# Optimization experiments

Hardware: AMD Instinct MI355X
Metric: run time of the kernel (lower is better)

The kernel has to match this reference:

```python
import jax, jax.numpy as jnp
import numpy as np
import math

D = 512      # d_model
HEADS = 16   # num_heads
HD = 32      # head_dim
WS = 7       # window_size
KS = 8       # patch_size
S = 4        # spectral_stride


def dct_basis(n):
    k = np.arange(n, dtype=np.float64)[:, None]
    i = np.arange(n, dtype=np.float64)[None, :]
    B = np.cos(np.pi * (i + 0.5) * k / n)
    B[0, :] *= 1.0 / np.sqrt(2.0)
    B = B * np.sqrt(2.0 / n)
    return jnp.asarray(B, dtype=jnp.float32)


def setup_inputs() -> dict:
    key = jax.random.key(0)
    ks = jax.random.split(key, 24)
    Bb, H, W = 4, 112, 112
    N = H * W
    w = lambda k, shape: jax.random.normal(k, shape, jnp.float32) * 0.02
    return {
        'tokens': jax.random.normal(ks[0], (Bb, N, D), jnp.float32),
        'patches': jax.random.normal(ks[1], (Bb, 3 * KS * KS, N), jnp.float32),
        'Wq': w(ks[2], (D, D)), 'bq': w(ks[3], (D,)),
        'Wk': w(ks[4], (D, D)), 'bk': w(ks[5], (D,)),
        'Wv': w(ks[6], (D, D)), 'bv': w(ks[7], (D,)),
        'Wo': w(ks[8], (D, D)), 'bo': w(ks[9], (D,)),
        'Wsp': w(ks[10], (3 * KS * KS, D)), 'bsp': w(ks[11], (D,)),
        'Wsq': w(ks[12], (D, D)), 'bsq': w(ks[13], (D,)),
        'Wsk': w(ks[14], (D, D)), 'bsk': w(ks[15], (D,)),
        'Wsv': w(ks[16], (D, D)), 'bsv': w(ks[17], (D,)),
        'Wso': w(ks[18], (D, D)), 'bso': w(ks[19], (D,)),
        'alpha': jnp.asarray(0.5, jnp.float32),
        'H': H, 'W': W,
    }


def reference(tokens, patches, Wq, bq, Wk, bk, Wv, bv, Wo, bo,
              Wsp, bsp, Wsq, bsq, Wsk, bsk, Wsv, bsv, Wso, bso,
              alpha, H, W):
    B, N, d = tokens.shape
    # ---- local windowed multi-head attention ----
    ws = WS
    pad_h = (-H) % ws
    pad_w = (-W) % ws
    x = tokens.reshape(B, H, W, d)
    if pad_h or pad_w:
        x = jnp.pad(x, ((0, 0), (0, pad_h), (0, pad_w), (0, 0)))
    Hp, Wp = H + pad_h, W + pad_w
    nh, nw_ = Hp // ws, Wp // ws
    xw = x.reshape(B, nh, ws, nw_, ws, d).transpose(0, 1, 3, 2, 4, 5)
    xw = xw.reshape(B * nh * nw_, ws * ws, d)  # (nw, 49, d)
    nw, L, _ = xw.shape
    q = (xw @ Wq + bq).reshape(nw, L, HEADS, HD)
    k = (xw @ Wk + bk).reshape(nw, L, HEADS, HD)
    v = (xw @ Wv + bv).reshape(nw, L, HEADS, HD)
    scale = 1.0 / math.sqrt(HD)
    attn = jax.nn.softmax(jnp.einsum('nqhd,nkhd->nhqk', q, k) * scale, axis=-1)
    o = jnp.einsum('nhqk,nkhd->nqhd', attn, v).reshape(nw, L, d)
    o = o @ Wo + bo
    o = o.reshape(B, nh, nw_, ws, ws, d).transpose(0, 1, 3, 2, 4, 5).reshape(B, Hp, Wp, d)
    sp_out = o[:, :H, :W, :].reshape(B, N, d)
    # ---- DCT on raw patches -> spectral descriptors ----
    Bm = dct_basis(KS)
    p = patches.reshape(B, 3, KS, KS, N)
    Fc = jnp.einsum('ij,bcjkn->bcikn', Bm, p)
    Fc = jnp.einsum('bcijn,jk->bcikn', Fc, Bm)  # right-multiply by Bm^T transposed back
    spec_desc = Fc.reshape(B, 3 * KS * KS, N).transpose(0, 2, 1) @ Wsp + bsp  # (B,N,d)
    # ---- strided global spectral attention + nearest upsample ----
    spec_hw = spec_desc.reshape(B, H, W, d)
    sd = spec_hw[:, ::S, ::S, :]
    Hs, Ws = sd.shape[1], sd.shape[2]
    sd = sd.reshape(B, Hs * Ws, d)
    qs = sd @ Wsq + bsq
    ks_ = sd @ Wsk + bsk
    vs = sd @ Wsv + bsv
    a = jax.nn.softmax(jnp.einsum('bqd,bkd->bqk', qs, ks_) / math.sqrt(d), axis=-1)
    so = jnp.einsum('bqk,bkd->bqd', a, vs) @ Wso + bso
    so = so.reshape(B, Hs, Ws, d)
    ri = (jnp.arange(H) * Hs) // H  # torch nearest: floor(i*in/out)
    ci = (jnp.arange(W) * Ws) // W
    spec_out = so[:, ri][:, :, ci].reshape(B, N, d)
    # ---- fuse + residual + layernorm (no affine) ----
    al = jax.nn.sigmoid(alpha)
    out = tokens + al * sp_out + (1.0 - al) * spec_out
    mu = out.mean(-1, keepdims=True)
    var = ((out - mu) ** 2).mean(-1, keepdims=True)
    return (out - mu) / jnp.sqrt(var + 1e-5)
```

## Files before the change

kernel.cpp:

```cpp
#include <hip/hip_runtime.h>

typedef unsigned short u16;
typedef __attribute__((ext_vector_type(4))) float f32x4;
typedef __attribute__((ext_vector_type(8))) short bf16x8;

#define AS1 __attribute__((address_space(1)))
#define AS3 __attribute__((address_space(3)))
#define GLL(gp, lp) __builtin_amdgcn_global_load_lds((const AS1 void*)(gp), (AS3 void*)(lp), 16, 0, 0)

__device__ __forceinline__ float b2f(u16 v) { return __uint_as_float(((unsigned)v) << 16); }
__device__ __forceinline__ u16 f2b(float f) {
  unsigned u = __float_as_uint(f);
  u += 0x7fffu + ((u >> 16) & 1u);
  return (u16)(u >> 16);
}
__device__ __forceinline__ unsigned pack2(float a, float b) {
  return (unsigned)f2b(a) | ((unsigned)f2b(b) << 16);
}
__device__ __forceinline__ float blo(unsigned u) { return __uint_as_float(u << 16); }
__device__ __forceinline__ float bhi(unsigned u) { return __uint_as_float(u & 0xffff0000u); }

__global__ __launch_bounds__(512, 6) void gemm_bt512(
    const u16* __restrict__ A, int lda,
    const u16* __restrict__ Bt, int ldb,
    const float* __restrict__ bias, void* __restrict__ Cv, int ldc,
    int M, int N, int K, int c_bf16)
{
  __shared__ __align__(16) u16 ldsA[128 * 64];
  __shared__ __align__(16) u16 ldsB[128 * 64];
  int tid = threadIdx.x;
  int wid = tid >> 6, lane = tid & 63;
  int lm = lane & 15, lg = lane >> 4;
  int wm = wid >> 2, wn = wid & 3;

  int nbx = gridDim.x;
  int lin = blockIdx.y * nbx + blockIdx.x;
  int nwg = nbx * gridDim.y;
  int qc = nwg >> 3, rc = nwg & 7;
  int xcd = lin & 7, pos = lin >> 3;
  int nlin = (xcd < rc ? xcd * (qc + 1) : rc * (qc + 1) + (xcd - rc) * qc) + pos;
  int bx = nlin % nbx, by = nlin / nbx;

  int row0 = by << 7;
  int col0 = bx << 7;
  int wr = wm << 6, wc = wn << 5;

  const u16* pA[2];
  const u16* pB[2];
  int ldso[2];
#pragma unroll
  for (int q = 0; q < 2; ++q) {
    int o = (q << 13) + (tid << 4);
    int r = o >> 7;
    int cs = (o >> 4) & 7;
    int cl = cs ^ (r & 7);
    int ar = row0 + r; ar = ar < M ? ar : M - 1;
    int br = col0 + r; br = br < N ? br : N - 1;
    pA[q] = A + (size_t)ar * lda + (cl << 3);
    pB[q] = Bt + (size_t)br * ldb + (cl << 3);
    ldso[q] = o >> 1;
  }

  f32x4 acc[4][2];
#pragma unroll
  for (int i = 0; i < 4; ++i)
#pragma unroll
    for (int j = 0; j < 2; ++j) { f32x4 z = {0.f, 0.f, 0.f, 0.f}; acc[i][j] = z; }

  int nt = K >> 6;
  for (int t = 0; t < nt; ++t) {
#pragma unroll
    for (int q = 0; q < 2; ++q) {
      GLL(pA[q], ldsA + ldso[q]);
      GLL(pB[q], ldsB + ldso[q]);
      pA[q] += 64; pB[q] += 64;
    }
    __syncthreads();
#pragma unroll
    for (int kk = 0; kk < 2; ++kk) {
      bf16x8 af[4], bg[2];
#pragma unroll
      for (int mi = 0; mi < 4; ++mi) {
        int r = wr + (mi << 4) + lm;
        int cs = ((kk << 2) + lg) ^ (r & 7);
        af[mi] = *(const bf16x8*)(ldsA + (r << 6) + (cs << 3));
      }
#pragma unroll
      for (int ni = 0; ni < 2; ++ni) {
        int r = wc + (ni << 4) + lm;
        int cs = ((kk << 2) + lg) ^ (r & 7);
        bg[ni] = *(const bf16x8*)(ldsB + (r << 6) + (cs << 3));
      }
#pragma unroll
      for (int mi = 0; mi < 4; ++mi)
#pragma unroll
        for (int ni = 0; ni < 2; ++ni)
          acc[mi][ni] = __builtin_amdgcn_mfma_f32_16x16x32_bf16(af[mi], bg[ni], acc[mi][ni], 0, 0, 0);
    }
    __syncthreads();
  }

#pragma unroll
  for (int mi = 0; mi < 4; ++mi) {
    int rb = row0 + wr + (mi << 4) + (lg << 2);
#pragma unroll
    for (int ni = 0; ni < 2; ++ni) {
      int c = col0 + wc + (ni << 4) + lm;
      float bv = (bias && c < N) ? bias[c] : 0.f;
#pragma unroll
      for (int j = 0; j < 4; ++j) {
        int r = rb + j;
        if (r < M && c < N) {
          float v = acc[mi][ni][j] + bv;
          if (c_bf16) ((u16*)Cv)[(size_t)r * ldc + c] = f2b(v);
          else ((float*)Cv)[(size_t)r * ldc + c] = v;
        }
      }
    }
  }
}

__global__ __launch_bounds__(256, 6) void gemm_bt(
    const u16* __restrict__ A, int lda, long sAb,
    const u16* __restrict__ Bt, int ldb, long sBb,
    const float* __restrict__ bias, void* __restrict__ Cv, int ldc, long sCb,
    int M, int N, int K, int c_bf16)
{
  __shared__ __align__(16) u16 ldsA[128 * 64];
  __shared__ __align__(16) u16 ldsB[64 * 64];
  int tid = threadIdx.x;
  int wid = tid >> 6, lane = tid & 63;

  int nbx = gridDim.x;
  int lin = blockIdx.y * nbx + blockIdx.x;
  int nwg = nbx * gridDim.y;
  int qc = nwg >> 3, rc = nwg & 7;
  int xcd = lin & 7, pos = lin >> 3;
  int nlin = (xcd < rc ? xcd * (qc + 1) : rc * (qc + 1) + (xcd - rc) * qc) + pos;
  int bx = nlin % nbx, by = nlin / nbx;

  int row0 = by << 7;
  int col0 = bx << 6;
  int bz = blockIdx.z;
  A += (size_t)bz * sAb;
  Bt += (size_t)bz * sBb;
  int wr = (wid >> 1) << 6, wc = (wid & 1) << 5;

  const u16* pA[4];
  const u16* pB[2];
  int ldsoA[4], ldsoB[2];
#pragma unroll
  for (int q = 0; q < 4; ++q) {
    int inst = (wid << 2) + q;
    int o = (inst << 10) + (lane << 4);
    int r = o >> 7;
    int cs = (o >> 4) & 7;
    int cl = cs ^ (r & 7);
    int ar = row0 + r; ar = ar < M ? ar : M - 1;
    pA[q] = A + (size_t)ar * lda + (cl << 3);
    ldsoA[q] = inst << 9;
  }
#pragma unroll
  for (int q = 0; q < 2; ++q) {
    int inst = (wid << 1) + q;
    int o = (inst << 10) + (lane << 4);
    int r = o >> 7;
    int cs = (o >> 4) & 7;
    int cl = cs ^ (r & 7);
    int br = col0 + r; br = br < N ? br : N - 1;
    pB[q] = Bt + (size_t)br * ldb + (cl << 3);
    ldsoB[q] = inst << 9;
  }

  f32x4 acc[4][2];
#pragma unroll
  for (int i = 0; i < 4; ++i)
#pragma unroll
    for (int j = 0; j < 2; ++j) { f32x4 z = {0.f, 0.f, 0.f, 0.f}; acc[i][j] = z; }

  int nt = K >> 6;
  for (int t = 0; t < nt; ++t) {
#pragma unroll
    for (int q = 0; q < 4; ++q) { GLL(pA[q], ldsA + ldsoA[q]); pA[q] += 64; }
#pragma unroll
    for (int q = 0; q < 2; ++q) { GLL(pB[q], ldsB + ldsoB[q]); pB[q] += 64; }
    __syncthreads();
#pragma unroll
    for (int kk = 0; kk < 2; ++kk) {
      bf16x8 af[4], bg[2];
#pragma unroll
      for (int mi = 0; mi < 4; ++mi) {
        int r = wr + (mi << 4) + (lane & 15);
        int cs = ((kk << 2) + (lane >> 4)) ^ (r & 7);
        af[mi] = *(const bf16x8*)(ldsA + (r << 6) + (cs << 3));
      }
#pragma unroll
      for (int ni = 0; ni < 2; ++ni) {
        int r = wc + (ni << 4) + (lane & 15);
        int cs = ((kk << 2) + (lane >> 4)) ^ (r & 7);
        bg[ni] = *(const bf16x8*)(ldsB + (r << 6) + (cs << 3));
      }
#pragma unroll
      for (int mi = 0; mi < 4; ++mi)
#pragma unroll
        for (int ni = 0; ni < 2; ++ni)
          acc[mi][ni] = __builtin_amdgcn_mfma_f32_16x16x32_bf16(af[mi], bg[ni], acc[mi][ni], 0, 0, 0);
    }
    __syncthreads();
  }

#pragma unroll
  for (int mi = 0; mi < 4; ++mi) {
    int rb = row0 + wr + (mi << 4) + ((lane >> 4) << 2);
#pragma unroll
    for (int ni = 0; ni < 2; ++ni) {
      int c = col0 + wc + (ni << 4) + (lane & 15);
      float bv = (bias && c < N) ? bias[c] : 0.f;
#pragma unroll
      for (int j = 0; j < 4; ++j) {
        int r = rb + j;
        if (r < M && c < N) {
          float v = acc[mi][ni][j] + bv;
          if (c_bf16) ((u16*)Cv)[(size_t)bz * sCb + (size_t)r * ldc + c] = f2b(v);
          else ((float*)Cv)[(size_t)bz * sCb + (size_t)r * ldc + c] = v;
        }
      }
    }
  }
}

__global__ __launch_bounds__(256, 2) void win_attn_mfma(const u16* __restrict__ qkv, u16* __restrict__ oat)
{
  __shared__ __align__(16) u16 Pl[4][64 * 72];
  __shared__ __align__(16) u16 Vtl[4][32 * 72];
  int tid = threadIdx.x;
  int wid = tid >> 6, lane = tid & 63;
  int lm = lane & 15, lg = lane >> 4;
  int w = blockIdx.x;
  int b = w >> 8, wh = (w >> 4) & 15, ww = w & 15;
  int rowbase = (wh * 7) * 112 + ww * 7;
  u16* P = Pl[wid];
  u16* Vt = Vtl[wid];
  const u16* base = qkv + (size_t)b * 12544 * 1536;
  u16* ob = oat + (size_t)b * 12544 * 512;
  const float scale = 0.17677669529663687f;

  for (int hh = 0; hh < 4; ++hh) {
    int h = wid * 4 + hh;
    bf16x8 Qf[4], Kf[4];
#pragma unroll
    for (int mi = 0; mi < 4; ++mi) {
      int i = mi * 16 + lm; i = i < 49 ? i : 48;
      int q7 = (i * 147) >> 10;
      int n = rowbase + q7 * 112 + (i - q7 * 7);
      const u16* rp = base + (size_t)n * 1536 + h * 32 + lg * 8;
      Qf[mi] = *(const bf16x8*)(rp);
      Kf[mi] = *(const bf16x8*)(rp + 512);
    }
    {
      int j = lane;
      if (j < 49) {
        int q7 = (j * 147) >> 10;
        int n = rowbase + q7 * 112 + (j - q7 * 7);
        const uint4* vp = (const uint4*)(base + (size_t)n * 1536 + 1024 + h * 32);
#pragma unroll
        for (int t = 0; t < 4; ++t) {
          uint4 u = vp[t];
          Vt[(t * 8 + 0) * 72 + j] = (u16)(u.x & 0xffff); Vt[(t * 8 + 1) * 72 + j] = (u16)(u.x >> 16);
          Vt[(t * 8 + 2) * 72 + j] = (u16)(u.y & 0xffff); Vt[(t * 8 + 3) * 72 + j] = (u16)(u.y >> 16);
          Vt[(t * 8 + 4) * 72 + j] = (u16)(u.z & 0xffff); Vt[(t * 8 + 5) * 72 + j] = (u16)(u.z >> 16);
          Vt[(t * 8 + 6) * 72 + j] = (u16)(u.w & 0xffff); Vt[(t * 8 + 7) * 72 + j] = (u16)(u.w >> 16);
        }
      } else {
#pragma unroll
        for (int d = 0; d < 32; ++d) Vt[d * 72 + j] = 0;
      }
    }
    f32x4 S[4][4];
#pragma unroll
    for (int mi = 0; mi < 4; ++mi)
#pragma unroll
      for (int nj = 0; nj < 4; ++nj) { f32x4 z = {0.f, 0.f, 0.f, 0.f}; S[mi][nj] = z; }
#pragma unroll
    for (int mi = 0; mi < 4; ++mi)
#pragma unroll
      for (int nj = 0; nj < 4; ++nj)
        S[mi][nj] = __builtin_amdgcn_mfma_f32_16x16x32_bf16(Qf[mi], Kf[nj], S[mi][nj], 0, 0, 0);
    float invv[4][4];
#pragma unroll
    for (int mi = 0; mi < 4; ++mi) {
#pragma unroll
      for (int reg = 0; reg < 4; ++reg) {
        float v0 = S[mi][0][reg], v1 = S[mi][1][reg], v2 = S[mi][2][reg], v3 = S[mi][3][reg];
        if (lm) v3 = -1e30f;
        float m = fmaxf(fmaxf(v0, v1), fmaxf(v2, v3));
#pragma unroll
        for (int o = 1; o < 16; o <<= 1) m = fmaxf(m, __shfl_xor(m, o));
        float e0 = __expf((v0 - m) * scale);
        float e1 = __expf((v1 - m) * scale);
        float e2 = __expf((v2 - m) * scale);
        float e3 = lm ? 0.f : __expf((v3 - m) * scale);
        float s = e0 + e1 + e2 + e3;
#pragma unroll
        for (int o = 1; o < 16; o <<= 1) s += __shfl_xor(s, o);
        invv[mi][reg] = 1.f / s;
        int r = mi * 16 + lg * 4 + reg;
        P[r * 72 + lm] = f2b(e0);
        P[r * 72 + 16 + lm] = f2b(e1);
        P[r * 72 + 32 + lm] = f2b(e2);
        P[r * 72 + 48 + lm] = f2b(e3);
      }
    }
    bf16x8 Vf[2][2];
#pragma unroll
    for (int dt = 0; dt < 2; ++dt) {
      Vf[dt][0] = *(const bf16x8*)(Vt + (dt * 16 + lm) * 72 + lg * 8);
      Vf[dt][1] = *(const bf16x8*)(Vt + (dt * 16 + lm) * 72 + 32 + lg * 8);
    }
    f32x4 O[4][2];
#pragma unroll
    for (int mi = 0; mi < 4; ++mi)
#pragma unroll
      for (int dt = 0; dt < 2; ++dt) { f32x4 z = {0.f, 0.f, 0.f, 0.f}; O[mi][dt] = z; }
#pragma unroll
    for (int mi = 0; mi < 4; ++mi) {
      bf16x8 Pf0 = *(const bf16x8*)(P + (mi * 16 + lm) * 72 + lg * 8);
      bf16x8 Pf1 = *(const bf16x8*)(P + (mi * 16 + lm) * 72 + 32 + lg * 8);
#pragma unroll
      for (int dt = 0; dt < 2; ++dt) {
        O[mi][dt] = __builtin_amdgcn_mfma_f32_16x16x32_bf16(Pf0, Vf[dt][0], O[mi][dt], 0, 0, 0);
        O[mi][dt] = __builtin_amdgcn_mfma_f32_16x16x32_bf16(Pf1, Vf[dt][1], O[mi][dt], 0, 0, 0);
      }
    }
#pragma unroll
    for (int mi = 0; mi < 4; ++mi)
#pragma unroll
      for (int reg = 0; reg < 4; ++reg) {
        int i = mi * 16 + lg * 4 + reg;
        if (i < 49) {
          int q7 = (i * 147) >> 10;
          int n = rowbase + q7 * 112 + (i - q7 * 7);
          float iv = invv[mi][reg];
          u16* op = ob + (size_t)n * 512 + h * 32 + lm;
          op[0] = f2b(O[mi][0][reg] * iv);
          op[16] = f2b(O[mi][1][reg] * iv);
        }
      }
  }
}

__global__ __launch_bounds__(192) void dct_f2(const float* __restrict__ patches, u16* __restrict__ F2)
{
  __shared__ float pv[192];
  __shared__ float Bm[64];
  int blk = blockIdx.x;
  int b = blk / 784, rem = blk % 784;
  int n = ((rem / 28) * 4) * 112 + (rem % 28) * 4;
  int t = threadIdx.x;
  if (t < 64) {
    int k = t >> 3, ii = t & 7;
    float v = cosf(3.14159265358979323846f * (ii + 0.5f) * (float)k * 0.125f) * 0.5f;
    if (k == 0) v *= 0.70710678118654752f;
    Bm[t] = v;
  }
  pv[t] = patches[((size_t)b * 192 + t) * 12544 + n];
  __syncthreads();
  int c = t >> 6, fi = (t >> 3) & 7, fk = t & 7;
  float acc = 0.f;
#pragma unroll
  for (int mm = 0; mm < 8; ++mm) {
    float g = 0.f;
#pragma unroll
    for (int jj = 0; jj < 8; ++jj) g += pv[c * 64 + mm * 8 + jj] * Bm[jj * 8 + fk];
    acc += Bm[fi * 8 + mm] * g;
  }
  F2[(size_t)blk * 192 + t] = f2b(acc);
}

__global__ __launch_bounds__(256) void spec_softmax(const float* __restrict__ S, u16* __restrict__ P)
{
  __shared__ float red[4];
  int row = blockIdx.x;
  const float* sr = S + (size_t)row * 784;
  u16* pr = P + (size_t)row * 832;
  int t = threadIdx.x;
  int lane = t & 63, wid = t >> 6;
  float v0 = sr[t];
  float v1 = sr[t + 256];
  float v2 = (t < 272) ? sr[t + 512] : -1e30f;
  float m = fmaxf(fmaxf(v0, v1), v2);
#pragma unroll
  for (int ofs = 32; ofs > 0; ofs >>= 1) m = fmaxf(m, __shfl_xor(m, ofs));
  if (lane == 0) red[wid] = m;
  __syncthreads();
  m = fmaxf(fmaxf(red[0], red[1]), fmaxf(red[2], red[3]));
  __syncthreads();
  const float scale = 0.044194173824159216f;
  float e0 = __expf((v0 - m) * scale);
  float e1 = __expf((v1 - m) * scale);
  float e2 = (t < 272) ? __expf((v2 - m) * scale) : 0.f;
  float sum = e0 + e1 + e2;
#pragma unroll
  for (int ofs = 32; ofs > 0; ofs >>= 1) sum += __shfl_xor(sum, ofs);
  if (lane == 0) red[wid] = sum;
  __syncthreads();
  sum = red[0] + red[1] + red[2] + red[3];
  float inv = 1.f / sum;
  pr[t] = f2b(e0 * inv);
  pr[t + 256] = f2b(e1 * inv);
  if (t < 272) pr[t + 512] = f2b(e2 * inv);
  else if (t < 320) pr[t + 512] = 0;
}

__global__ __launch_bounds__(256) void transV(const u16* __restrict__ qkvs, u16* __restrict__ Vt)
{
  int idx = blockIdx.x * 256 + threadIdx.x;
  int k = idx % 832;
  int rest = idx / 832;
  int n = rest % 512, b = rest / 512;
  u16 v = 0;
  if (k < 784) v = qkvs[((size_t)(b * 784 + k)) * 1536 + 1024 + n];
  Vt[idx] = v;
}

__global__ __launch_bounds__(256) void combine_ln(
    const float* __restrict__ tokens, const u16* __restrict__ sp,
    const float* __restrict__ so, const float* __restrict__ alpha,
    float* __restrict__ out)
{
  int nidx = blockIdx.x;
  int b = nidx / 12544, pos = nidx % 12544;
  int i = pos / 112, j = pos % 112;
  const float* tr = tokens + (size_t)nidx * 512;
  const u16* sr = sp + (size_t)nidx * 512;
  const float* qr = so + (size_t)(b * 784 + (i >> 2) * 28 + (j >> 2)) * 512;
  float al = 1.f / (1.f + __expf(-alpha[0]));
  float be = 1.f - al;
  int t = threadIdx.x;
  float x0 = tr[t] + al * b2f(sr[t]) + be * qr[t];
  float x1 = tr[t + 256] + al * b2f(sr[t + 256]) + be * qr[t + 256];
  float s = x0 + x1, ss = x0 * x0 + x1 * x1;
#pragma unroll
  for (int ofs = 32; ofs > 0; ofs >>= 1) { s += __shfl_xor(s, ofs); ss += __shfl_xor(ss, ofs); }
  __shared__ float rs[4], rq[4];
  int lane = t & 63, wid = t >> 6;
  if (lane == 0) { rs[wid] = s; rq[wid] = ss; }
  __syncthreads();
  s = rs[0] + rs[1] + rs[2] + rs[3];
  ss = rq[0] + rq[1] + rq[2] + rq[3];
  float mu = s * 0.001953125f;
  float var = ss * 0.001953125f - mu * mu;
  float rstd = rsqrtf(var + 1e-5f);
  float* orow = out + (size_t)nidx * 512;
  orow[t] = (x0 - mu) * rstd;
  orow[t + 256] = (x1 - mu) * rstd;
}

__global__ __launch_bounds__(256) void transT(const float* __restrict__ src, u16* __restrict__ dst, int K, int Nc)
{
  int idx = blockIdx.x * 256 + threadIdx.x;
  if (idx >= K * Nc) return;
  int nn = idx / K, kk = idx % K;
  dst[idx] = f2b(src[(size_t)kk * Nc + nn]);
}

__global__ __launch_bounds__(256) void cvtbf(const float* __restrict__ src, u16* __restrict__ dst)
{
  size_t i = ((size_t)blockIdx.x * 256 + threadIdx.x) * 4;
  float4 v = *(const float4*)(src + i);
  uint2 u;
  u.x = pack2(v.x, v.y);
  u.y = pack2(v.z, v.w);
  *(uint2*)(dst + i) = u;
}

__global__ __launch_bounds__(256) void stack_bias(
    const float* bq_, const float* bk_, const float* bv_,
    const float* bsq_, const float* bsk_, const float* bsv_,
    float* bqkv, float* bsqkv)
{
  int i = blockIdx.x * 256 + threadIdx.x;
  if (i >= 1536) return;
  int r = i & 511;
  bqkv[i]  = (i < 512) ? bq_[r]  : (i < 1024) ? bk_[r]  : bv_[r];
  bsqkv[i] = (i < 512) ? bsq_[r] : (i < 1024) ? bsk_[r] : bsv_[r];
}

extern "C" void kernel_launch(void* const* d_in, const int* in_sizes, int n_in,
                              void* d_out, int out_size, void* d_ws, size_t ws_size,
                              hipStream_t stream) {
  (void)in_sizes; (void)n_in; (void)out_size; (void)ws_size;
  const float* tokens = (const float*)d_in[0];
  const float* patches = (const float*)d_in[1];
  const float* Wq  = (const float*)d_in[2];
  const float* bq  = (const float*)d_in[3];
  const float* Wk  = (const float*)d_in[4];
  const float* bk  = (const float*)d_in[5];
  const float* Wv  = (const float*)d_in[6];
  const float* bv  = (const float*)d_in[7];
  const float* Wo  = (const float*)d_in[8];
  const float* bo  = (const float*)d_in[9];
  const float* Wsp = (const float*)d_in[10];
  const float* bsp = (const float*)d_in[11];
  const float* Wsq = (const float*)d_in[12];
  const float* bsq = (const float*)d_in[13];
  const float* Wsk = (const float*)d_in[14];
  const float* bsk = (const float*)d_in[15];
  const float* Wsv = (const float*)d_in[16];
  const float* bsv = (const float*)d_in[17];
  const float* Wso = (const float*)d_in[18];
  const float* bso = (const float*)d_in[19];
  const float* alpha = (const float*)d_in[20];
  float* out = (float*)d_out;

  char* ws = (char*)d_ws;
  u16* tokbf  = (u16*)ws;
  u16* qkv    = (u16*)(ws + 51380224);
  char* pp    = ws + 51380224 + 154140672;
  u16* WqkvT  = (u16*)pp; pp += 1572864;
  u16* WoT    = (u16*)pp; pp += 524288;
  u16* WsqkvT = (u16*)pp; pp += 1572864;
  u16* WsoT   = (u16*)pp; pp += 524288;
  u16* WspT   = (u16*)pp; pp += 196608;
  float* bqkv = (float*)pp; pp += 6144;
  float* bsqkv= (float*)pp; pp += 6144;
  u16* F2b    = (u16*)pp; pp += 1204224;
  u16* sd     = (u16*)pp; pp += 3211264;
  u16* qkvs   = (u16*)pp; pp += 9633792;
  u16* sopre  = (u16*)pp; pp += 3211264;
  float* sofin= (float*)pp; pp += 6422528;

  float* Sbuf = (float*)tokbf;
  u16* Pbuf   = (u16*)(ws + 9834496);
  u16* Vt     = (u16*)(ws + 9834496 + 5218304);

  cvtbf<<<25088, 256, 0, stream>>>(tokens, tokbf);
  transT<<<1024, 256, 0, stream>>>(Wq, WqkvT, 512, 512);
  transT<<<1024, 256, 0, stream>>>(Wk, WqkvT + 262144, 512, 512);
  transT<<<1024, 256, 0, stream>>>(Wv, WqkvT + 524288, 512, 512);
  transT<<<1024, 256, 0, stream>>>(Wo, WoT, 512, 512);
  transT<<<1024, 256, 0, stream>>>(Wsq, WsqkvT, 512, 512);
  transT<<<1024, 256, 0, stream>>>(Wsk, WsqkvT + 262144, 512, 512);
  transT<<<1024, 256, 0, stream>>>(Wsv, WsqkvT + 524288, 512, 512);
  transT<<<1024, 256, 0, stream>>>(Wso, WsoT, 512, 512);
  transT<<<384, 256, 0, stream>>>(Wsp, WspT, 192, 512);
  stack_bias<<<6, 256, 0, stream>>>(bq, bk, bv, bsq, bsk, bsv, bqkv, bsqkv);

  gemm_bt512<<<dim3(12, 392), 512, 0, stream>>>(tokbf, 512, WqkvT, 512, bqkv, qkv, 1536, 50176, 1536, 512, 1);
  win_attn_mfma<<<1024, 256, 0, stream>>>(qkv, tokbf);
  gemm_bt<<<dim3(8, 392), 256, 0, stream>>>(tokbf, 512, 0, WoT, 512, 0, bo, qkv, 512, 0, 50176, 512, 512, 1);

  dct_f2<<<3136, 192, 0, stream>>>(patches, F2b);
  gemm_bt<<<dim3(8, 25), 256, 0, stream>>>(F2b, 192, 0, WspT, 192, 0, bsp, sd, 512, 0, 3136, 512, 192, 1);
  gemm_bt<<<dim3(24, 25), 256, 0, stream>>>(sd, 512, 0, WsqkvT, 512, 0, bsqkv, qkvs, 1536, 0, 3136, 1536, 512, 1);
  gemm_bt<<<dim3(13, 7, 4), 256, 0, stream>>>(qkvs, 1536, (long)784 * 1536, qkvs + 512, 1536, (long)784 * 1536,
                                              nullptr, Sbuf, 784, (long)784 * 784, 784, 784, 512, 0);
  spec_softmax<<<3136, 256, 0, stream>>>(Sbuf, Pbuf);
  transV<<<6656, 256, 0, stream>>>(qkvs, Vt);
  gemm_bt<<<dim3(8, 7, 4), 256, 0, stream>>>(Pbuf, 832, (long)784 * 832, Vt, 832, (long)512 * 832,
                                             nullptr, sopre, 512, (long)784 * 512, 784, 512, 832, 1);
  gemm_bt<<<dim3(8, 25), 256, 0, stream>>>(sopre, 512, 0, WsoT, 512, 0, bso, sofin, 512, 0, 3136, 512, 512, 0);

  combine_ln<<<50176, 256, 0, stream>>>(tokens, qkv, sofin, alpha, out);
}
```

Before: 459.4 us.

## Split window attention across heads, vectorize combine_ln, batch weight transposes

The window attention kernel now launches one block per (window, head-quarter), so each wave handles a single head instead of looping over four. This gives four times as many blocks to spread across compute units. combine_ln now uses float2 and packed bf16 loads and stores per thread, replacing scalar strided accesses. The eight 512x512 weight transposes are merged into one launch that selects its source and destination by blockIdx.z, which cuts launch overhead. Splitting by head means each block reloads the window row addresses and does more per-block setup.

```diff
diff --git a/kernel.cpp b/kernel.cpp
--- a/kernel.cpp
+++ b/kernel.cpp
@@ -236,7 +236,9 @@
   int tid = threadIdx.x;
   int wid = tid >> 6, lane = tid & 63;
   int lm = lane & 15, lg = lane >> 4;
-  int w = blockIdx.x;
+  int blk = blockIdx.x;
+  int w = blk >> 2, hq = blk & 3;
+  int h = hq * 4 + wid;
   int b = w >> 8, wh = (w >> 4) & 15, ww = w & 15;
   int rowbase = (wh * 7) * 112 + ww * 7;
   u16* P = Pl[wid];
@@ -245,108 +247,105 @@
   u16* ob = oat + (size_t)b * 12544 * 512;
   const float scale = 0.17677669529663687f;
 
-  for (int hh = 0; hh < 4; ++hh) {
-    int h = wid * 4 + hh;
-    bf16x8 Qf[4], Kf[4];
-#pragma unroll
-    for (int mi = 0; mi < 4; ++mi) {
-      int i = mi * 16 + lm; i = i < 49 ? i : 48;
-      int q7 = (i * 147) >> 10;
-      int n = rowbase + q7 * 112 + (i - q7 * 7);
-      const u16* rp = base + (size_t)n * 1536 + h * 32 + lg * 8;
-      Qf[mi] = *(const bf16x8*)(rp);
-      Kf[mi] = *(const bf16x8*)(rp + 512);
-    }
-    {
-      int j = lane;
-      if (j < 49) {
-        int q7 = (j * 147) >> 10;
-        int n = rowbase + q7 * 112 + (j - q7 * 7);
-        const uint4* vp = (const uint4*)(base + (size_t)n * 1536 + 1024 + h * 32);
-#pragma unroll
-        for (int t = 0; t < 4; ++t) {
-          uint4 u = vp[t];
-          Vt[(t * 8 + 0) * 72 + j] = (u16)(u.x & 0xffff); Vt[(t * 8 + 1) * 72 + j] = (u16)(u.x >> 16);
-          Vt[(t * 8 + 2) * 72 + j] = (u16)(u.y & 0xffff); Vt[(t * 8 + 3) * 72 + j] = (u16)(u.y >> 16);
-          Vt[(t * 8 + 4) * 72 + j] = (u16)(u.z & 0xffff); Vt[(t * 8 + 5) * 72 + j] = (u16)(u.z >> 16);
-          Vt[(t * 8 + 6) * 72 + j] = (u16)(u.w & 0xffff); Vt[(t * 8 + 7) * 72 + j] = (u16)(u.w >> 16);
-        }
-      } else {
-#pragma unroll
-        for (int d = 0; d < 32; ++d) Vt[d * 72 + j] = 0;
-      }
-    }
-    f32x4 S[4][4];
-#pragma unroll
-    for (int mi = 0; mi < 4; ++mi)
-#pragma unroll
-      for (int nj = 0; nj < 4; ++nj) { f32x4 z = {0.f, 0.f, 0.f, 0.f}; S[mi][nj] = z; }
-#pragma unroll
-    for (int mi = 0; mi < 4; ++mi)
-#pragma unroll
-      for (int nj = 0; nj < 4; ++nj)
-        S[mi][nj] = __builtin_amdgcn_mfma_f32_16x16x32_bf16(Qf[mi], Kf[nj], S[mi][nj], 0, 0, 0);
-    float invv[4][4];
-#pragma unroll
-    for (int mi = 0; mi < 4; ++mi) {
-#pragma unroll
-      for (int reg = 0; reg < 4; ++reg) {
-        float v0 = S[mi][0][reg], v1 = S[mi][1][reg], v2 = S[mi][2][reg], v3 = S[mi][3][reg];
-        if (lm) v3 = -1e30f;
-        float m = fmaxf(fmaxf(v0, v1), fmaxf(v2, v3));
-#pragma unroll
-        for (int o = 1; o < 16; o <<= 1) m = fmaxf(m, __shfl_xor(m, o));
-        float e0 = __expf((v0 - m) * scale);
-        float e1 = __expf((v1 - m) * scale);
-        float e2 = __expf((v2 - m) * scale);
-        float e3 = lm ? 0.f : __expf((v3 - m) * scale);
-        float s = e0 + e1 + e2 + e3;
-#pragma unroll
-        for (int o = 1; o < 16; o <<= 1) s += __shfl_xor(s, o);
-        invv[mi][reg] = 1.f / s;
-        int r = mi * 16 + lg * 4 + reg;
-        P[r * 72 + lm] = f2b(e0);
-        P[r * 72 + 16 + lm] = f2b(e1);
-        P[r * 72 + 32 + lm] = f2b(e2);
-        P[r * 72 + 48 + lm] = f2b(e3);
-      }
-    }
-    bf16x8 Vf[2][2];
+  bf16x8 Qf[4], Kf[4];
+#pragma unroll
+  for (int mi = 0; mi < 4; ++mi) {
+    int i = mi * 16 + lm; i = i < 49 ? i : 48;
+    int q7 = (i * 147) >> 10;
+    int n = rowbase + q7 * 112 + (i - q7 * 7);
+    const u16* rp = base + (size_t)n * 1536 + h * 32 + lg * 8;
+    Qf[mi] = *(const bf16x8*)(rp);
+    Kf[mi] = *(const bf16x8*)(rp + 512);
+  }
+  {
+    int j = lane;
+    if (j < 49) {
+      int q7 = (j * 147) >> 10;
+      int n = rowbase + q7 * 112 + (j - q7 * 7);
+      const uint4* vp = (const uint4*)(base + (size_t)n * 1536 + 1024 + h * 32);
+#pragma unroll
+      for (int t = 0; t < 4; ++t) {
+        uint4 u = vp[t];
+        Vt[(t * 8 + 0) * 72 + j] = (u16)(u.x & 0xffff); Vt[(t * 8 + 1) * 72 + j] = (u16)(u.x >> 16);
+        Vt[(t * 8 + 2) * 72 + j] = (u16)(u.y & 0xffff); Vt[(t * 8 + 3) * 72 + j] = (u16)(u.y >> 16);
+        Vt[(t * 8 + 4) * 72 + j] = (u16)(u.z & 0xffff); Vt[(t * 8 + 5) * 72 + j] = (u16)(u.z >> 16);
+        Vt[(t * 8 + 6) * 72 + j] = (u16)(u.w & 0xffff); Vt[(t * 8 + 7) * 72 + j] = (u16)(u.w >> 16);
+      }
+    } else {
+#pragma unroll
+      for (int d = 0; d < 32; ++d) Vt[d * 72 + j] = 0;
+    }
+  }
+  f32x4 S[4][4];
+#pragma unroll
+  for (int mi = 0; mi < 4; ++mi)
+#pragma unroll
+    for (int nj = 0; nj < 4; ++nj) { f32x4 z = {0.f, 0.f, 0.f, 0.f}; S[mi][nj] = z; }
+#pragma unroll
+  for (int mi = 0; mi < 4; ++mi)
+#pragma unroll
+    for (int nj = 0; nj < 4; ++nj)
+      S[mi][nj] = __builtin_amdgcn_mfma_f32_16x16x32_bf16(Qf[mi], Kf[nj], S[mi][nj], 0, 0, 0);
+  float invv[4][4];
+#pragma unroll
+  for (int mi = 0; mi < 4; ++mi) {
+#pragma unroll
+    for (int reg = 0; reg < 4; ++reg) {
+      float v0 = S[mi][0][reg], v1 = S[mi][1][reg], v2 = S[mi][2][reg], v3 = S[mi][3][reg];
+      if (lm) v3 = -1e30f;
+      float m = fmaxf(fmaxf(v0, v1), fmaxf(v2, v3));
+#pragma unroll
+      for (int o = 1; o < 16; o <<= 1) m = fmaxf(m, __shfl_xor(m, o));
+      float e0 = __expf((v0 - m) * scale);
+      float e1 = __expf((v1 - m) * scale);
+      float e2 = __expf((v2 - m) * scale);
+      float e3 = lm ? 0.f : __expf((v3 - m) * scale);
+      float s = e0 + e1 + e2 + e3;
+#pragma unroll
+      for (int o = 1; o < 16; o <<= 1) s += __shfl_xor(s, o);
+      invv[mi][reg] = 1.f / s;
+      int r = mi * 16 + lg * 4 + reg;
+      P[r * 72 + lm] = f2b(e0);
+      P[r * 72 + 16 + lm] = f2b(e1);
+      P[r * 72 + 32 + lm] = f2b(e2);
+      P[r * 72 + 48 + lm] = f2b(e3);
+    }
+  }
+  bf16x8 Vf[2][2];
+#pragma unroll
+  for (int dt = 0; dt < 2; ++dt) {
+    Vf[dt][0] = *(const bf16x8*)(Vt + (dt * 16 + lm) * 72 + lg * 8);
+    Vf[dt][1] = *(const bf16x8*)(Vt + (dt * 16 + lm) * 72 + 32 + lg * 8);
+  }
+  f32x4 O[4][2];
+#pragma unroll
+  for (int mi = 0; mi < 4; ++mi)
+#pragma unroll
+    for (int dt = 0; dt < 2; ++dt) { f32x4 z = {0.f, 0.f, 0.f, 0.f}; O[mi][dt] = z; }
+#pragma unroll
+  for (int mi = 0; mi < 4; ++mi) {
+    bf16x8 Pf0 = *(const bf16x8*)(P + (mi * 16 + lm) * 72 + lg * 8);
+    bf16x8 Pf1 = *(const bf16x8*)(P + (mi * 16 + lm) * 72 + 32 + lg * 8);
 #pragma unroll
     for (int dt = 0; dt < 2; ++dt) {
-      Vf[dt][0] = *(const bf16x8*)(Vt + (dt * 16 + lm) * 72 + lg * 8);
-      Vf[dt][1] = *(const bf16x8*)(Vt + (dt * 16 + lm) * 72 + 32 + lg * 8);
-    }
-    f32x4 O[4][2];
-#pragma unroll
-    for (int mi = 0; mi < 4; ++mi)
-#pragma unroll
-      for (int dt = 0; dt < 2; ++dt) { f32x4 z = {0.f, 0.f, 0.f, 0.f}; O[mi][dt] = z; }
-#pragma unroll
-    for (int mi = 0; mi < 4; ++mi) {
-      bf16x8 Pf0 = *(const bf16x8*)(P + (mi * 16 + lm) * 72 + lg * 8);
-      bf16x8 Pf1 = *(const bf16x8*)(P + (mi * 16 + lm) * 72 + 32 + lg * 8);
-#pragma unroll
-      for (int dt = 0; dt < 2; ++dt) {
-        O[mi][dt] = __builtin_amdgcn_mfma_f32_16x16x32_bf16(Pf0, Vf[dt][0], O[mi][dt], 0, 0, 0);
-        O[mi][dt] = __builtin_amdgcn_mfma_f32_16x16x32_bf16(Pf1, Vf[dt][1], O[mi][dt], 0, 0, 0);
-      }
-    }
-#pragma unroll
-    for (int mi = 0; mi < 4; ++mi)
-#pragma unroll
-      for (int reg = 0; reg < 4; ++reg) {
-        int i = mi * 16 + lg * 4 + reg;
-        if (i < 49) {
-          int q7 = (i * 147) >> 10;
-          int n = rowbase + q7 * 112 + (i - q7 * 7);
-          float iv = invv[mi][reg];
-          u16* op = ob + (size_t)n * 512 + h * 32 + lm;
-          op[0] = f2b(O[mi][0][reg] * iv);
-          op[16] = f2b(O[mi][1][reg] * iv);
-        }
-      }
-  }
+      O[mi][dt] = __builtin_amdgcn_mfma_f32_16x16x32_bf16(Pf0, Vf[dt][0], O[mi][dt], 0, 0, 0);
+      O[mi][dt] = __builtin_amdgcn_mfma_f32_16x16x32_bf16(Pf1, Vf[dt][1], O[mi][dt], 0, 0, 0);
+    }
+  }
+#pragma unroll
+  for (int mi = 0; mi < 4; ++mi)
+#pragma unroll
+    for (int reg = 0; reg < 4; ++reg) {
+      int i = mi * 16 + lg * 4 + reg;
+      if (i < 49) {
+        int q7 = (i * 147) >> 10;
+        int n = rowbase + q7 * 112 + (i - q7 * 7);
+        float iv = invv[mi][reg];
+        u16* op = ob + (size_t)n * 512 + h * 32 + lm;
+        op[0] = f2b(O[mi][0][reg] * iv);
+        op[16] = f2b(O[mi][1][reg] * iv);
+      }
+    }
 }
 
 __global__ __launch_bounds__(192) void dct_f2(const float* __restrict__ patches, u16* __restrict__ F2)
@@ -437,8 +436,11 @@
   float al = 1.f / (1.f + __expf(-alpha[0]));
   float be = 1.f - al;
   int t = threadIdx.x;
-  float x0 = tr[t] + al * b2f(sr[t]) + be * qr[t];
-  float x1 = tr[t + 256] + al * b2f(sr[t + 256]) + be * qr[t + 256];
+  float2 tv = *(const float2*)(tr + 2 * t);
+  unsigned sv = *(const unsigned*)(sr + 2 * t);
+  float2 qv = *(const float2*)(qr + 2 * t);
+  float x0 = tv.x + al * blo(sv) + be * qv.x;
+  float x1 = tv.y + al * bhi(sv) + be * qv.y;
   float s = x0 + x1, ss = x0 * x0 + x1 * x1;
 #pragma unroll
   for (int ofs = 32; ofs > 0; ofs >>= 1) { s += __shfl_xor(s, ofs); ss += __shfl_xor(ss, ofs); }
@@ -451,9 +453,31 @@
   float mu = s * 0.001953125f;
   float var = ss * 0.001953125f - mu * mu;
   float rstd = rsqrtf(var + 1e-5f);
-  float* orow = out + (size_t)nidx * 512;
-  orow[t] = (x0 - mu) * rstd;
-  orow[t + 256] = (x1 - mu) * rstd;
+  float2 ov;
+  ov.x = (x0 - mu) * rstd;
+  ov.y = (x1 - mu) * rstd;
+  *(float2*)(out + (size_t)nidx * 512 + 2 * t) = ov;
+}
+
+__global__ __launch_bounds__(256) void transT8(
+    const float* s0, const float* s1, const float* s2, const float* s3,
+    const float* s4, const float* s5, const float* s6, const float* s7,
+    u16* d0, u16* d1, u16* d2, u16* d3, u16* d4, u16* d5, u16* d6, u16* d7)
+{
+  const float* src; u16* dst;
+  switch (blockIdx.z) {
+    case 0: src = s0; dst = d0; break;
+    case 1: src = s1; dst = d1; break;
+    case 2: src = s2; dst = d2; break;
+    case 3: src = s3; dst = d3; break;
+    case 4: src = s4; dst = d4; break;
+    case 5: src = s5; dst = d5; break;
+    case 6: src = s6; dst = d6; break;
+    default: src = s7; dst = d7; break;
+  }
+  int idx = blockIdx.x * 256 + threadIdx.x;
+  int nn = idx >> 9, kk = idx & 511;
+  dst[idx] = f2b(src[(kk << 9) + nn]);
 }
 
 __global__ __launch_bounds__(256) void transT(const float* __restrict__ src, u16* __restrict__ dst, int K, int Nc)
@@ -535,19 +559,15 @@
   u16* Vt     = (u16*)(ws + 9834496 + 5218304);
 
   cvtbf<<<25088, 256, 0, stream>>>(tokens, tokbf);
-  transT<<<1024, 256, 0, stream>>>(Wq, WqkvT, 512, 512);
-  transT<<<1024, 256, 0, stream>>>(Wk, WqkvT + 262144, 512, 512);
-  transT<<<1024, 256, 0, stream>>>(Wv, WqkvT + 524288, 512, 512);
-  transT<<<1024, 256, 0, stream>>>(Wo, WoT, 512, 512);
-  transT<<<1024, 256, 0, stream>>>(Wsq, WsqkvT, 512, 512);
-  transT<<<1024, 256, 0, stream>>>(Wsk, WsqkvT + 262144, 512, 512);
-  transT<<<1024, 256, 0, stream>>>(Wsv, WsqkvT + 524288, 512, 512);
-  transT<<<1024, 256, 0, stream>>>(Wso, WsoT, 512, 512);
+  transT8<<<dim3(1024, 1, 8), 256, 0, stream>>>(
+      Wq, Wk, Wv, Wo, Wsq, Wsk, Wsv, Wso,
+      WqkvT, WqkvT + 262144, WqkvT + 524288, WoT,
+      WsqkvT, WsqkvT + 262144, WsqkvT + 524288, WsoT);
   transT<<<384, 256, 0, stream>>>(Wsp, WspT, 192, 512);
   stack_bias<<<6, 256, 0, stream>>>(bq, bk, bv, bsq, bsk, bsv, bqkv, bsqkv);
 
   gemm_bt512<<<dim3(12, 392), 512, 0, stream>>>(tokbf, 512, WqkvT, 512, bqkv, qkv, 1536, 50176, 1536, 512, 1);
-  win_attn_mfma<<<1024, 256, 0, stream>>>(qkv, tokbf);
+  win_attn_mfma<<<4096, 256, 0, stream>>>(qkv, tokbf);
   gemm_bt<<<dim3(8, 392), 256, 0, stream>>>(tokbf, 512, 0, WoT, 512, 0, bo, qkv, 512, 0, 50176, 512, 512, 1);
 
   dct_f2<<<3136, 192, 0, stream>>>(patches, F2b);
```

Measured after the change: 435.4 us, median of 2. 1.06x faster.
